# Kernel tuning notes

Hardware: AMD Instinct MI355X
Metric: run time of the kernel (lower is better)

Reference implementation:

```python
import jax, jax.numpy as jnp
import numpy as np

DECAY = 0.99
EPS = 1e-5


def setup_inputs() -> dict:
    key = jax.random.key(0)
    k1, k2 = jax.random.split(key)
    inp = jax.random.normal(k1, (32, 64, 64, 64), dtype=jnp.float32)  # [B,H,W,dim]
    embed = jax.random.normal(k2, (64, 512), dtype=jnp.float32)       # [dim, n_embed]
    cluster_size = jnp.zeros((512,), dtype=jnp.float32)
    embed_avg = embed  # buffer initialized as embed.clone() in torch
    return {"input": inp, "embed": embed, "cluster_size": cluster_size, "embed_avg": embed_avg}


def reference(input, embed, cluster_size, embed_avg):
    dim, n_embed = embed.shape
    flatten = input.reshape(-1, dim)  # [N, dim]

    # pairwise squared distances via ||f||^2 - 2 f.E + ||E||^2 -> [N, n_embed]
    dist = ((flatten ** 2).sum(1, keepdims=True)
            - 2.0 * flatten @ embed
            + (embed ** 2).sum(0, keepdims=True))
    embed_ind_flat = jnp.argmin(dist, axis=1)  # [N] (== argmax of -dist)

    # codebook lookup (F.embedding on embed.T)
    quantize = jnp.take(embed.T, embed_ind_flat, axis=0).reshape(input.shape)

    # EMA stats: one-hot sum and one-hot @ flatten expressed as scatter-adds
    ones = jnp.ones_like(embed_ind_flat, dtype=flatten.dtype)
    embed_onehot_sum = jax.ops.segment_sum(ones, embed_ind_flat, num_segments=n_embed)      # [n_embed]
    embed_sum = jax.ops.segment_sum(flatten, embed_ind_flat, num_segments=n_embed).T       # [dim, n_embed]

    new_cluster_size = cluster_size * DECAY + (1.0 - DECAY) * embed_onehot_sum
    new_embed_avg = embed_avg * DECAY + (1.0 - DECAY) * embed_sum
    n = new_cluster_size.sum()
    cs = (new_cluster_size + EPS) / (n + n_embed * EPS) * n
    new_embed = new_embed_avg / cs[None, :]

    diff = ((jax.lax.stop_gradient(quantize) - input) ** 2).mean()
    quantize_st = input + jax.lax.stop_gradient(quantize - input)  # straight-through
    embed_ind = embed_ind_flat.reshape(input.shape[:-1])

    return (quantize_st, diff, embed_ind, new_cluster_size, new_embed_avg, new_embed)
```

## Files before the change

kernel.cpp:

```cpp
#include <hip/hip_runtime.h>

typedef __attribute__((ext_vector_type(8))) short short8_t;
typedef __attribute__((ext_vector_type(4))) float f32x4;

#define N_ROWS   131072
#define DIM      64
#define NE       512
#define DECAYF   0.99f
#define OMDECAY  0.01f
#define EPSF     1e-5f
#define GAP_THR  0.02f

#define Q_OFF    0
#define DIFF_OFF 8388608
#define IND_OFF  8388609
#define CS_OFF   8519681
#define AVG_OFF  8520193
#define EMB_OFF  8552961

#define WS_ET      0
#define WS_ENORM   32768
#define WS_EN64    33280
#define WS_CSDIV   34304
#define WS_DIFF    34816
#define WS_RCNT    34817
#define WS_IDX     34818
#define WS_RLIST   165890
#define WS_BH      296964
#define WS_BL      313348
#define WS_HIST    329732
#define WS_BINBASE 330244
#define WS_CURSOR  330756
#define WS_SORTED  331268
#define WS_ACCUM   462340

__device__ __forceinline__ ushort f32_to_bf16_rn(float f) {
    unsigned u = __float_as_uint(f);
    unsigned r = (u + 0x7FFFu + ((u >> 16) & 1u)) >> 16;
    return (ushort)r;
}
__device__ __forceinline__ float bf16_to_f32(ushort h) {
    return __uint_as_float(((unsigned)h) << 16);
}

__global__ __launch_bounds__(512) void prep1_kernel(const float* __restrict__ embed,
                                                    float* __restrict__ ws) {
    const int d = blockIdx.x;
    const int c = threadIdx.x;
    float v = embed[d * NE + c];
    ws[WS_ET + c * DIM + d] = v;

    ushort hb = f32_to_bf16_rn(v);
    float  lf = v - bf16_to_f32(hb);
    ushort lb = f32_to_bf16_rn(lf);

    const int T  = c >> 4;
    const int n  = c & 15;
    const int s  = d >> 5;
    const int k8 = (d >> 3) & 3;
    const int j  = d & 7;
    const int l  = k8 * 16 + n;
    const int idx = (T * 2 + s) * 512 + l * 8 + j;
    ((ushort*)(ws + WS_BH))[idx] = hb;
    ((ushort*)(ws + WS_BL))[idx] = lb;

    if (d == 0 && c == 0) {
        ws[WS_DIFF] = 0.0f;
        ((int*)ws)[WS_RCNT] = 0;
    }
    if (d == 1) ((int*)ws)[WS_HIST + c] = 0;
    ws[WS_ACCUM + blockIdx.x * 512 + threadIdx.x] = 0.0f;
}

__global__ __launch_bounds__(256) void prep2_kernel(float* __restrict__ ws) {
    const int jcode = blockIdx.x * 4 + (threadIdx.x >> 6);
    const int d     = threadIdx.x & 63;
    float v = ws[WS_ET + jcode * DIM + d];
    double sq = (double)v * (double)v;
    #pragma unroll
    for (int off = 32; off > 0; off >>= 1) sq += __shfl_down(sq, off, 64);
    if (d == 0) {
        ws[WS_ENORM + jcode] = (float)sq;
        ((double*)(ws + WS_EN64))[jcode] = sq;
    }
}

__global__ __launch_bounds__(256) void dist_kernel(const float* __restrict__ input,
                                                   float* __restrict__ ws) {
    const int tid  = threadIdx.x;
    const int lane = tid & 63;
    const int wv   = tid >> 6;
    const int r0   = blockIdx.x * 128 + wv * 32;
    const int n15  = lane & 15;
    const int koff = (lane >> 4) * 8;

    short8_t Ahi[2][2], Alo[2][2];
    #pragma unroll
    for (int sub = 0; sub < 2; sub++) {
        const float* rp = input + (size_t)(r0 + sub * 16 + n15) * DIM + koff;
        #pragma unroll
        for (int s = 0; s < 2; s++) {
            float4 x0 = *(const float4*)(rp + s * 32);
            float4 x1 = *(const float4*)(rp + s * 32 + 4);
            float xf[8] = {x0.x, x0.y, x0.z, x0.w, x1.x, x1.y, x1.z, x1.w};
            short8_t h, l;
            #pragma unroll
            for (int e = 0; e < 8; e++) {
                ushort hb = f32_to_bf16_rn(xf[e]);
                float  lf = xf[e] - bf16_to_f32(hb);
                ushort lb = f32_to_bf16_rn(lf);
                h[e] = (short)hb;
                l[e] = (short)lb;
            }
            Ahi[sub][s] = h;
            Alo[sub][s] = l;
        }
    }

    const ushort* bhp = (const ushort*)(ws + WS_BH) + lane * 8;
    const ushort* blp = (const ushort*)(ws + WS_BL) + lane * 8;

    float m1[8], m2[8];
    int   j1[8];
    #pragma unroll
    for (int i = 0; i < 8; i++) { m1[i] = 3.4e38f; m2[i] = 3.4e38f; j1[i] = 0; }

    #pragma unroll 2
    for (int T = 0; T < 32; T++) {
        short8_t Bh0 = *(const short8_t*)(bhp + T * 1024);
        short8_t Bh1 = *(const short8_t*)(bhp + T * 1024 + 512);
        short8_t Bl0 = *(const short8_t*)(blp + T * 1024);
        short8_t Bl1 = *(const short8_t*)(blp + T * 1024 + 512);

        f32x4 aa = {0.f, 0.f, 0.f, 0.f};
        f32x4 ab = {0.f, 0.f, 0.f, 0.f};
        aa = __builtin_amdgcn_mfma_f32_16x16x32_bf16(Ahi[0][0], Bh0, aa, 0, 0, 0);
        ab = __builtin_amdgcn_mfma_f32_16x16x32_bf16(Ahi[1][0], Bh0, ab, 0, 0, 0);
        aa = __builtin_amdgcn_mfma_f32_16x16x32_bf16(Alo[0][0], Bh0, aa, 0, 0, 0);
        ab = __builtin_amdgcn_mfma_f32_16x16x32_bf16(Alo[1][0], Bh0, ab, 0, 0, 0);
        aa = __builtin_amdgcn_mfma_f32_16x16x32_bf16(Ahi[0][0], Bl0, aa, 0, 0, 0);
        ab = __builtin_amdgcn_mfma_f32_16x16x32_bf16(Ahi[1][0], Bl0, ab, 0, 0, 0);
        aa = __builtin_amdgcn_mfma_f32_16x16x32_bf16(Ahi[0][1], Bh1, aa, 0, 0, 0);
        ab = __builtin_amdgcn_mfma_f32_16x16x32_bf16(Ahi[1][1], Bh1, ab, 0, 0, 0);
        aa = __builtin_amdgcn_mfma_f32_16x16x32_bf16(Alo[0][1], Bh1, aa, 0, 0, 0);
        ab = __builtin_amdgcn_mfma_f32_16x16x32_bf16(Alo[1][1], Bh1, ab, 0, 0, 0);
        aa = __builtin_amdgcn_mfma_f32_16x16x32_bf16(Ahi[0][1], Bl1, aa, 0, 0, 0);
        ab = __builtin_amdgcn_mfma_f32_16x16x32_bf16(Ahi[1][1], Bl1, ab, 0, 0, 0);

        const float en = ws[WS_ENORM + T * 16 + n15];
        const int   jc = T * 16 + n15;
        #pragma unroll
        for (int q = 0; q < 4; q++) {
            float da = fmaf(-2.0f, aa[q], en);
            m2[q]    = fminf(m2[q], fmaxf(m1[q], da));
            j1[q]    = (da < m1[q]) ? jc : j1[q];
            m1[q]    = fminf(m1[q], da);
            float db = fmaf(-2.0f, ab[q], en);
            m2[q+4]  = fminf(m2[q+4], fmaxf(m1[q+4], db));
            j1[q+4]  = (db < m1[q+4]) ? jc : j1[q+4];
            m1[q+4]  = fminf(m1[q+4], db);
        }
    }

    #pragma unroll
    for (int off = 1; off < 16; off <<= 1) {
        #pragma unroll
        for (int i = 0; i < 8; i++) {
            float b1 = __shfl_xor(m1[i], off, 64);
            float b2 = __shfl_xor(m2[i], off, 64);
            int   bj = __shfl_xor(j1[i], off, 64);
            float a1 = m1[i];
            float nm2 = fminf(fminf(m2[i], b2), fmaxf(a1, b1));
            bool takeB = (b1 < a1) || (b1 == a1 && bj < j1[i]);
            m1[i] = takeB ? b1 : a1;
            j1[i] = takeB ? bj : j1[i];
            m2[i] = nm2;
        }
    }

    if (n15 == 0) {
        #pragma unroll
        for (int i = 0; i < 8; i++) {
            int sub = i >> 2, q = i & 3;
            int r = r0 + sub * 16 + (lane >> 4) * 4 + q;
            ((int*)ws)[WS_IDX + r] = j1[i];
            if (m2[i] - m1[i] < GAP_THR) {
                int pos = atomicAdd((int*)ws + WS_RCNT, 1);
                ((int*)ws)[WS_RLIST + pos] = r;
            }
        }
    }
}

__global__ __launch_bounds__(64) void refine_kernel(const float* __restrict__ input,
                                                    float* __restrict__ ws) {
    __shared__ float rowf[DIM];
    const int cnt  = ((const int*)ws)[WS_RCNT];
    const int lane = threadIdx.x;
    const double* en64 = (const double*)(ws + WS_EN64);
    for (int ii = blockIdx.x; ii < cnt; ii += 512) {
        const int r = ((const int*)ws)[WS_RLIST + ii];
        __syncthreads();
        rowf[lane] = input[(size_t)r * DIM + lane];
        __syncthreads();
        double bd = 1e300;
        int    bj = 0x7fffffff;
        for (int kk = 0; kk < 8; kk++) {
            int j = kk * 64 + lane;
            const float* ep = ws + WS_ET + j * DIM;
            double s = 0.0;
            #pragma unroll 8
            for (int d = 0; d < DIM; d++)
                s = fma((double)ep[d], (double)rowf[d], s);
            double dist = en64[j] - 2.0 * s;
            if (dist < bd || (dist == bd && j < bj)) { bd = dist; bj = j; }
        }
        #pragma unroll
        for (int off = 32; off > 0; off >>= 1) {
            double od = __shfl_down(bd, off, 64);
            int    oj = __shfl_down(bj, off, 64);
            if (od < bd || (od == bd && oj < bj)) { bd = od; bj = oj; }
        }
        if (lane == 0) ((int*)ws)[WS_IDX + r] = bj;
    }
}

__global__ __launch_bounds__(256) void quantize_kernel(const float* __restrict__ input,
                                                       float* __restrict__ ws,
                                                       float* __restrict__ out) {
    __shared__ int hist[NE];
    __shared__ float wsum[4];
    const int tid = threadIdx.x;
    for (int e = tid; e < NE; e += 256) hist[e] = 0;
    __syncthreads();

    const int lane = tid & 63;
    const int wv   = tid >> 6;
    const int rsub = lane >> 4;
    const int d4   = (lane & 15) * 4;
    const int base = blockIdx.x * 256;
    float dacc = 0.0f;

    #pragma unroll 4
    for (int it = 0; it < 16; it++) {
        int r = base + (it * 4 + wv) * 4 + rsub;
        int j = ((const int*)ws)[WS_IDX + r];
        float4 in4 = *(const float4*)(input + (size_t)r * DIM + d4);
        float4 q4  = *(const float4*)(ws + WS_ET + j * DIM + d4);
        *(float4*)(out + Q_OFF + (size_t)r * DIM + d4) = q4;
        float dx = q4.x - in4.x, dy = q4.y - in4.y, dz = q4.z - in4.z, dw = q4.w - in4.w;
        dacc = fmaf(dx, dx, fmaf(dy, dy, fmaf(dz, dz, fmaf(dw, dw, dacc))));
        if ((lane & 15) == 0) {
            atomicAdd(&hist[j], 1);
            out[IND_OFF + r] = (float)j;
        }
    }
    __syncthreads();

    for (int e = tid; e < NE; e += 256) {
        int h = hist[e];
        if (h) atomicAdd((int*)ws + WS_HIST + e, h);
    }

    #pragma unroll
    for (int off = 32; off > 0; off >>= 1) dacc += __shfl_down(dacc, off, 64);
    if (lane == 0) wsum[wv] = dacc;
    __syncthreads();
    if (tid == 0)
        atomicAdd(&ws[WS_DIFF], wsum[0] + wsum[1] + wsum[2] + wsum[3]);
}

__global__ __launch_bounds__(512) void scan_kernel(const float* __restrict__ cluster_size,
                                                   float* __restrict__ ws,
                                                   float* __restrict__ out) {
    __shared__ int wsums[8];
    const int t    = threadIdx.x;
    const int lane = t & 63;
    const int wv   = t >> 6;
    const int v    = ((const int*)ws)[WS_HIST + t];
    int x = v;
    #pragma unroll
    for (int off = 1; off < 64; off <<= 1) {
        int y = __shfl_up(x, off, 64);
        if (lane >= off) x += y;
    }
    if (lane == 63) wsums[wv] = x;
    __syncthreads();
    int add = 0;
    for (int w = 0; w < wv; w++) add += wsums[w];
    const int excl = x + add - v;
    ((int*)ws)[WS_BINBASE + t] = excl;
    ((int*)ws)[WS_CURSOR + t]  = excl;
    out[CS_OFF + t] = fmaf(cluster_size[t], DECAYF, OMDECAY * (float)v);
}

__global__ __launch_bounds__(512) void finalize1_kernel(float* __restrict__ ws,
                                                        float* __restrict__ out) {
    __shared__ float red[8];
    const int t = threadIdx.x;
    float v = out[CS_OFF + t];
    float s = v;
    #pragma unroll
    for (int off = 32; off > 0; off >>= 1) s += __shfl_down(s, off, 64);
    if ((t & 63) == 0) red[t >> 6] = s;
    __syncthreads();
    float n = red[0] + red[1] + red[2] + red[3] + red[4] + red[5] + red[6] + red[7];
    ws[WS_CSDIV + t] = (v + EPSF) / (n + (float)NE * EPSF) * n;
    if (t == 0) out[DIFF_OFF] = ws[WS_DIFF] * (1.0f / 8388608.0f);
}

__global__ __launch_bounds__(256) void place_kernel(float* __restrict__ ws) {
    __shared__ int lhist[NE];
    __shared__ int lbase[NE];
    __shared__ int lcur[NE];
    const int tid  = threadIdx.x;
    const int base = blockIdx.x * 256;

    for (int e = tid; e < NE; e += 256) { lhist[e] = 0; lcur[e] = 0; }
    __syncthreads();

    const int r = base + tid;
    const int j = ((const int*)ws)[WS_IDX + r];
    atomicAdd(&lhist[j], 1);
    __syncthreads();

    for (int e = tid; e < NE; e += 256)
        if (lhist[e]) lbase[e] = atomicAdd((int*)ws + WS_CURSOR + e, lhist[e]);
    __syncthreads();

    const int pos = lbase[j] + atomicAdd(&lcur[j], 1);
    ((int*)ws)[WS_SORTED + pos] = r;
}

__global__ __launch_bounds__(64) void sum_kernel(const float* __restrict__ input,
                                                 float* __restrict__ ws) {
    const int lane = threadIdx.x;
    const int i0   = blockIdx.x * 64;

    const int rv = ((const int*)ws)[WS_SORTED + i0 + lane];
    const int jv = ((const int*)ws)[WS_IDX + rv];

    float acc  = 0.0f;
    int   jcur = __shfl(jv, 0, 64);

    for (int k = 0; k < 64; k += 4) {
        int r0 = __shfl(rv, k,     64);
        int r1 = __shfl(rv, k + 1, 64);
        int r2 = __shfl(rv, k + 2, 64);
        int r3 = __shfl(rv, k + 3, 64);
        float v0 = input[(size_t)r0 * DIM + lane];
        float v1 = input[(size_t)r1 * DIM + lane];
        float v2 = input[(size_t)r2 * DIM + lane];
        float v3 = input[(size_t)r3 * DIM + lane];
        int j0 = __shfl(jv, k,     64);
        int j1 = __shfl(jv, k + 1, 64);
        int j2 = __shfl(jv, k + 2, 64);
        int j3 = __shfl(jv, k + 3, 64);

        if (j0 != jcur) { atomicAdd(&ws[WS_ACCUM + jcur * DIM + lane], acc); acc = 0.0f; jcur = j0; }
        acc += v0;
        if (j1 != jcur) { atomicAdd(&ws[WS_ACCUM + jcur * DIM + lane], acc); acc = 0.0f; jcur = j1; }
        acc += v1;
        if (j2 != jcur) { atomicAdd(&ws[WS_ACCUM + jcur * DIM + lane], acc); acc = 0.0f; jcur = j2; }
        acc += v2;
        if (j3 != jcur) { atomicAdd(&ws[WS_ACCUM + jcur * DIM + lane], acc); acc = 0.0f; jcur = j3; }
        acc += v3;
    }
    atomicAdd(&ws[WS_ACCUM + jcur * DIM + lane], acc);
}

__global__ __launch_bounds__(512) void emaout_kernel(const float* __restrict__ embed_avg,
                                                     const float* __restrict__ ws,
                                                     float* __restrict__ out) {
    const int e = blockIdx.x * 512 + threadIdx.x;
    const int d = e >> 9;
    const int j = e & (NE - 1);
    float s   = ws[WS_ACCUM + j * DIM + d];
    float avg = fmaf(embed_avg[e], DECAYF, OMDECAY * s);
    out[AVG_OFF + e] = avg;
    out[EMB_OFF + e] = avg / ws[WS_CSDIV + j];
}

extern "C" void kernel_launch(void* const* d_in, const int* in_sizes, int n_in,
                              void* d_out, int out_size, void* d_ws, size_t ws_size,
                              hipStream_t stream) {
    const float* input        = (const float*)d_in[0];
    const float* embed        = (const float*)d_in[1];
    const float* cluster_size = (const float*)d_in[2];
    const float* embed_avg    = (const float*)d_in[3];
    float* out = (float*)d_out;
    float* ws  = (float*)d_ws;

    prep1_kernel<<<64, 512, 0, stream>>>(embed, ws);
    prep2_kernel<<<128, 256, 0, stream>>>(ws);
    dist_kernel<<<N_ROWS / 128, 256, 0, stream>>>(input, ws);
    refine_kernel<<<512, 64, 0, stream>>>(input, ws);
    quantize_kernel<<<512, 256, 0, stream>>>(input, ws, out);
    scan_kernel<<<1, 512, 0, stream>>>(cluster_size, ws, out);
    finalize1_kernel<<<1, 512, 0, stream>>>(ws, out);
    place_kernel<<<512, 256, 0, stream>>>(ws);
    sum_kernel<<<N_ROWS / 64, 64, 0, stream>>>(input, ws);
    emaout_kernel<<<64, 512, 0, stream>>>(embed_avg, ws, out);
}
```

Measured before the change: 138.7 us.

## Fuse quantize output and diff into sorted sum pass, merge scan and finalize

The quantize gather, index write and squared-error accumulation move into the sorted-order sum kernel, so the input is read once instead of twice. A slim histogram kernel that reads four indices per thread replaces the old quantize kernel. The scan and finalize kernels merge into one launch, and the diff output moves to the EMA kernel. Refine now runs four rows per block with no block barriers and two FMA chains. The catch is that quantize rows are now written in scattered, sorted order with one float per lane, so stores are less coalesced than the old float4 row-major writes.

```diff
diff --git a/kernel.cpp b/kernel.cpp
--- a/kernel.cpp
+++ b/kernel.cpp
@@ -58,9 +58,9 @@
     const int n  = c & 15;
     const int s  = d >> 5;
     const int k8 = (d >> 3) & 3;
-    const int j  = d & 7;
+    const int jj = d & 7;
     const int l  = k8 * 16 + n;
-    const int idx = (T * 2 + s) * 512 + l * 8 + j;
+    const int idx = (T * 2 + s) * 512 + l * 8 + jj;
     ((ushort*)(ws + WS_BH))[idx] = hb;
     ((ushort*)(ws + WS_BL))[idx] = lb;
 
@@ -192,27 +192,29 @@
     }
 }
 
-__global__ __launch_bounds__(64) void refine_kernel(const float* __restrict__ input,
-                                                    float* __restrict__ ws) {
-    __shared__ float rowf[DIM];
+__global__ __launch_bounds__(256) void refine_kernel(const float* __restrict__ input,
+                                                     float* __restrict__ ws) {
+    __shared__ float rowf[4][DIM];
     const int cnt  = ((const int*)ws)[WS_RCNT];
-    const int lane = threadIdx.x;
+    const int lane = threadIdx.x & 63;
+    const int wv   = threadIdx.x >> 6;
     const double* en64 = (const double*)(ws + WS_EN64);
-    for (int ii = blockIdx.x; ii < cnt; ii += 512) {
+
+    for (int ii = blockIdx.x * 4 + wv; ii < cnt; ii += 2048) {
         const int r = ((const int*)ws)[WS_RLIST + ii];
-        __syncthreads();
-        rowf[lane] = input[(size_t)r * DIM + lane];
-        __syncthreads();
+        rowf[wv][lane] = input[(size_t)r * DIM + lane];
         double bd = 1e300;
         int    bj = 0x7fffffff;
         for (int kk = 0; kk < 8; kk++) {
             int j = kk * 64 + lane;
             const float* ep = ws + WS_ET + j * DIM;
-            double s = 0.0;
+            double s0 = 0.0, s1 = 0.0;
             #pragma unroll 8
-            for (int d = 0; d < DIM; d++)
-                s = fma((double)ep[d], (double)rowf[d], s);
-            double dist = en64[j] - 2.0 * s;
+            for (int d = 0; d < DIM; d += 2) {
+                s0 = fma((double)ep[d],     (double)rowf[wv][d],     s0);
+                s1 = fma((double)ep[d + 1], (double)rowf[wv][d + 1], s1);
+            }
+            double dist = en64[j] - 2.0 * (s0 + s1);
             if (dist < bd || (dist == bd && j < bj)) { bd = dist; bj = j; }
         }
         #pragma unroll
@@ -225,59 +227,37 @@
     }
 }
 
-__global__ __launch_bounds__(256) void quantize_kernel(const float* __restrict__ input,
-                                                       float* __restrict__ ws,
-                                                       float* __restrict__ out) {
+__global__ __launch_bounds__(256) void hist_kernel(float* __restrict__ ws) {
     __shared__ int hist[NE];
-    __shared__ float wsum[4];
     const int tid = threadIdx.x;
     for (int e = tid; e < NE; e += 256) hist[e] = 0;
     __syncthreads();
 
-    const int lane = tid & 63;
-    const int wv   = tid >> 6;
-    const int rsub = lane >> 4;
-    const int d4   = (lane & 15) * 4;
-    const int base = blockIdx.x * 256;
-    float dacc = 0.0f;
-
-    #pragma unroll 4
-    for (int it = 0; it < 16; it++) {
-        int r = base + (it * 4 + wv) * 4 + rsub;
-        int j = ((const int*)ws)[WS_IDX + r];
-        float4 in4 = *(const float4*)(input + (size_t)r * DIM + d4);
-        float4 q4  = *(const float4*)(ws + WS_ET + j * DIM + d4);
-        *(float4*)(out + Q_OFF + (size_t)r * DIM + d4) = q4;
-        float dx = q4.x - in4.x, dy = q4.y - in4.y, dz = q4.z - in4.z, dw = q4.w - in4.w;
-        dacc = fmaf(dx, dx, fmaf(dy, dy, fmaf(dz, dz, fmaf(dw, dw, dacc))));
-        if ((lane & 15) == 0) {
-            atomicAdd(&hist[j], 1);
-            out[IND_OFF + r] = (float)j;
-        }
-    }
+    const int4 j4 = *((const int4*)((const int*)ws + WS_IDX) + blockIdx.x * 256 + tid);
+    atomicAdd(&hist[j4.x], 1);
+    atomicAdd(&hist[j4.y], 1);
+    atomicAdd(&hist[j4.z], 1);
+    atomicAdd(&hist[j4.w], 1);
     __syncthreads();
 
     for (int e = tid; e < NE; e += 256) {
         int h = hist[e];
         if (h) atomicAdd((int*)ws + WS_HIST + e, h);
     }
-
-    #pragma unroll
-    for (int off = 32; off > 0; off >>= 1) dacc += __shfl_down(dacc, off, 64);
-    if (lane == 0) wsum[wv] = dacc;
-    __syncthreads();
-    if (tid == 0)
-        atomicAdd(&ws[WS_DIFF], wsum[0] + wsum[1] + wsum[2] + wsum[3]);
-}
-
-__global__ __launch_bounds__(512) void scan_kernel(const float* __restrict__ cluster_size,
-                                                   float* __restrict__ ws,
-                                                   float* __restrict__ out) {
+}
+
+__global__ __launch_bounds__(512) void scanfin_kernel(const float* __restrict__ cluster_size,
+                                                      float* __restrict__ ws,
+                                                      float* __restrict__ out) {
     __shared__ int wsums[8];
+    __shared__ float red[8];
     const int t    = threadIdx.x;
     const int lane = t & 63;
     const int wv   = t >> 6;
     const int v    = ((const int*)ws)[WS_HIST + t];
+    const float csnew = fmaf(cluster_size[t], DECAYF, OMDECAY * (float)v);
+    out[CS_OFF + t] = csnew;
+
     int x = v;
     #pragma unroll
     for (int off = 1; off < 64; off <<= 1) {
@@ -285,28 +265,21 @@
         if (lane >= off) x += y;
     }
     if (lane == 63) wsums[wv] = x;
-    __syncthreads();
+
+    float s = csnew;
+    #pragma unroll
+    for (int off = 32; off > 0; off >>= 1) s += __shfl_down(s, off, 64);
+    if (lane == 0) red[wv] = s;
+    __syncthreads();
+
     int add = 0;
     for (int w = 0; w < wv; w++) add += wsums[w];
     const int excl = x + add - v;
     ((int*)ws)[WS_BINBASE + t] = excl;
     ((int*)ws)[WS_CURSOR + t]  = excl;
-    out[CS_OFF + t] = fmaf(cluster_size[t], DECAYF, OMDECAY * (float)v);
-}
-
-__global__ __launch_bounds__(512) void finalize1_kernel(float* __restrict__ ws,
-                                                        float* __restrict__ out) {
-    __shared__ float red[8];
-    const int t = threadIdx.x;
-    float v = out[CS_OFF + t];
-    float s = v;
-    #pragma unroll
-    for (int off = 32; off > 0; off >>= 1) s += __shfl_down(s, off, 64);
-    if ((t & 63) == 0) red[t >> 6] = s;
-    __syncthreads();
+
     float n = red[0] + red[1] + red[2] + red[3] + red[4] + red[5] + red[6] + red[7];
-    ws[WS_CSDIV + t] = (v + EPSF) / (n + (float)NE * EPSF) * n;
-    if (t == 0) out[DIFF_OFF] = ws[WS_DIFF] * (1.0f / 8388608.0f);
+    ws[WS_CSDIV + t] = (csnew + EPSF) / (n + (float)NE * EPSF) * n;
 }
 
 __global__ __launch_bounds__(256) void place_kernel(float* __restrict__ ws) {
@@ -332,15 +305,18 @@
     ((int*)ws)[WS_SORTED + pos] = r;
 }
 
-__global__ __launch_bounds__(64) void sum_kernel(const float* __restrict__ input,
-                                                 float* __restrict__ ws) {
-    const int lane = threadIdx.x;
-    const int i0   = blockIdx.x * 64;
+__global__ __launch_bounds__(256) void sum_kernel(const float* __restrict__ input,
+                                                  float* __restrict__ ws,
+                                                  float* __restrict__ out) {
+    const int lane = threadIdx.x & 63;
+    const int wv   = threadIdx.x >> 6;
+    const int i0   = (blockIdx.x * 4 + wv) * 64;
 
     const int rv = ((const int*)ws)[WS_SORTED + i0 + lane];
     const int jv = ((const int*)ws)[WS_IDX + rv];
 
     float acc  = 0.0f;
+    float dacc = 0.0f;
     int   jcur = __shfl(jv, 0, 64);
 
     for (int k = 0; k < 64; k += 4) {
@@ -357,6 +333,26 @@
         int j2 = __shfl(jv, k + 2, 64);
         int j3 = __shfl(jv, k + 3, 64);
 
+        float q0 = ws[WS_ET + j0 * DIM + lane];
+        float q1 = ws[WS_ET + j1 * DIM + lane];
+        float q2 = ws[WS_ET + j2 * DIM + lane];
+        float q3 = ws[WS_ET + j3 * DIM + lane];
+
+        out[Q_OFF + (size_t)r0 * DIM + lane] = q0;
+        out[Q_OFF + (size_t)r1 * DIM + lane] = q1;
+        out[Q_OFF + (size_t)r2 * DIM + lane] = q2;
+        out[Q_OFF + (size_t)r3 * DIM + lane] = q3;
+
+        float d0 = q0 - v0, d1 = q1 - v1, d2 = q2 - v2, d3 = q3 - v3;
+        dacc = fmaf(d0, d0, fmaf(d1, d1, fmaf(d2, d2, fmaf(d3, d3, dacc))));
+
+        if (lane == 0) {
+            out[IND_OFF + r0] = (float)j0;
+            out[IND_OFF + r1] = (float)j1;
+            out[IND_OFF + r2] = (float)j2;
+            out[IND_OFF + r3] = (float)j3;
+        }
+
         if (j0 != jcur) { atomicAdd(&ws[WS_ACCUM + jcur * DIM + lane], acc); acc = 0.0f; jcur = j0; }
         acc += v0;
         if (j1 != jcur) { atomicAdd(&ws[WS_ACCUM + jcur * DIM + lane], acc); acc = 0.0f; jcur = j1; }
@@ -367,6 +363,10 @@
         acc += v3;
     }
     atomicAdd(&ws[WS_ACCUM + jcur * DIM + lane], acc);
+
+    #pragma unroll
+    for (int off = 1; off < 64; off <<= 1) dacc += __shfl_xor(dacc, off, 64);
+    if (lane == 0) atomicAdd(&ws[WS_DIFF], dacc);
 }
 
 __global__ __launch_bounds__(512) void emaout_kernel(const float* __restrict__ embed_avg,
@@ -379,6 +379,7 @@
     float avg = fmaf(embed_avg[e], DECAYF, OMDECAY * s);
     out[AVG_OFF + e] = avg;
     out[EMB_OFF + e] = avg / ws[WS_CSDIV + j];
+    if (e == 0) out[DIFF_OFF] = ws[WS_DIFF] * (1.0f / 8388608.0f);
 }
 
 extern "C" void kernel_launch(void* const* d_in, const int* in_sizes, int n_in,
@@ -394,11 +395,10 @@
     prep1_kernel<<<64, 512, 0, stream>>>(embed, ws);
     prep2_kernel<<<128, 256, 0, stream>>>(ws);
     dist_kernel<<<N_ROWS / 128, 256, 0, stream>>>(input, ws);
-    refine_kernel<<<512, 64, 0, stream>>>(input, ws);
-    quantize_kernel<<<512, 256, 0, stream>>>(input, ws, out);
-    scan_kernel<<<1, 512, 0, stream>>>(cluster_size, ws, out);
-    finalize1_kernel<<<1, 512, 0, stream>>>(ws, out);
+    refine_kernel<<<512, 256, 0, stream>>>(input, ws);
+    hist_kernel<<<128, 256, 0, stream>>>(ws);
+    scanfin_kernel<<<1, 512, 0, stream>>>(cluster_size, ws, out);
     place_kernel<<<512, 256, 0, stream>>>(ws);
-    sum_kernel<<<N_ROWS / 64, 64, 0, stream>>>(input, ws);
+    sum_kernel<<<512, 256, 0, stream>>>(input, ws, out);
     emaout_kernel<<<64, 512, 0, stream>>>(embed_avg, ws, out);
 }
```

Measured after the change: 132.7 us. 1.05x faster.
